# Performance work log

Hardware: AMD Instinct MI355X
Metric: run time of the kernel (lower is better)

Reference implementation:

```python
import jax, jax.numpy as jnp
import numpy as np

B, C, T = 8, 256, 8192
CALC, H = 256, 4
D = CALC // H  # head dim = 64
EPS = 1e-5


def setup_inputs() -> dict:
    key = jax.random.key(0)
    ks = jax.random.split(key, 5)
    return {
        "x": jax.random.normal(ks[0], (B, C, T), dtype=jnp.float32),
        "W_prenet": jax.random.normal(ks[1], (3 * CALC, C), dtype=jnp.float32) * 0.05,
        "W_proj": jax.random.normal(ks[2], (C, CALC), dtype=jnp.float32) * 0.05,
        "b_proj": jax.random.normal(ks[3], (C,), dtype=jnp.float32) * 0.05,
        "scale": jax.random.normal(ks[4], (1,), dtype=jnp.float32),
        "gamma": jnp.ones((C,), dtype=jnp.float32),
        "beta": jnp.zeros((C,), dtype=jnp.float32),
    }


def reference(x, W_prenet, W_proj, b_proj, scale, gamma, beta):
    residual = x
    # 1x1 conv prenet: [B, 3*CALC, T]
    h = jnp.einsum('oc,bct->bot', W_prenet, x)
    # split heads: channels grouped as H blocks of 3*D, then chunk into q/k/v of D each
    h = h.reshape(B, H, 3 * D, T)
    q = h[:, :, :D, :]            # [B,H,D,T]
    k = h[:, :, D:2 * D, :]
    v = h[:, :, 2 * D:, :]
    # softmax over time on keys (with the module's +1e-5 shift)
    k = jax.nn.softmax(k + EPS, axis=3)
    # keys @ values^T : [B,H,Dk,Dv]
    kv = jnp.einsum('bhdt,bhet->bhde', k, v)
    # kv^T @ queries  : [B,H,Dv,T]
    ctx = jnp.einsum('bhde,bhdt->bhet', kv, q)
    ctx = ctx.reshape(B, CALC, T)
    # 1x1 conv projection + bias
    out = jnp.einsum('oc,bct->bot', W_proj, ctx) + b_proj[None, :, None]
    out = scale * out  # learnable scalar gate
    # dropout is identity in eval mode
    out = out + residual
    # LayerNorm over channel axis with per-channel affine
    mean = jnp.mean(out, axis=1, keepdims=True)
    var = jnp.var(out, axis=1, keepdims=True)
    out = (out - mean) * jax.lax.rsqrt(var + EPS)
    out = out * gamma[None, :, None] + beta[None, :, None]
    return out
```

## Files before the change

### kernel.cpp

```cpp
#include <hip/hip_runtime.h>
#include <hip/hip_bf16.h>
#include <math.h>

#define BB 8
#define CC 256
#define TT 8192
#define EPSF 1e-5f

typedef short v8s __attribute__((ext_vector_type(8)));
typedef float v4f __attribute__((ext_vector_type(4)));

#define MFMA(a, b, c) __builtin_amdgcn_mfma_f32_16x16x32_bf16((a), (b), (c), 0, 0, 0)


#define OFF_WKV 0
#define OFF_WPJ 65536
#define OFF_UPART 98304
#define OFF_ZPART 8486912
#define OFF_KV 8617984
#define OFF_PT 8749056
#define OFF_MBF 9011200

__device__ __forceinline__ unsigned short f2bf(float f) {
  __hip_bfloat16 h = __float2bfloat16(f);
  return __builtin_bit_cast(unsigned short, h);
}
__device__ __forceinline__ float bf2f(unsigned short u) {
  return __bfloat162float(__builtin_bit_cast(__hip_bfloat16, u));
}
__device__ __forceinline__ unsigned int pack2(float lo, float hi) {
  return (unsigned int)f2bf(lo) | ((unsigned int)f2bf(hi) << 16);
}

__global__ void k0_pack(const float* __restrict__ Wpre,
                        const float* __restrict__ Wproj,
                        float* __restrict__ ws) {
  const int r = blockIdx.x;
  const int c = threadIdx.x;
  if (r < 512) {
    const int h = r >> 7, type = (r >> 6) & 1, d = r & 63;
    const int src = h * 192 + 64 + type * 64 + d;
    ((unsigned short*)(ws + OFF_WKV))[r * 256 + c] = f2bf(Wpre[(size_t)src * 256 + c]);
  } else {
    const int rr = r - 512;
    ((unsigned short*)(ws + OFF_WPJ))[rr * 256 + c] = f2bf(Wproj[(size_t)rr * 256 + c]);
  }
}

__global__ __launch_bounds__(512, 2) void k1_kv(const float* __restrict__ x,
                                                float* __restrict__ ws) {
  __shared__ unsigned short lds[20480];

  const int tid = threadIdx.x;
  const int w = tid >> 6, lane = tid & 63, q = lane >> 4, cl = lane & 15;
  const int h = w >> 1, type = w & 1;
  const int bi = blockIdx.x;
  const int b = bi >> 6, chunk = bi & 63;
  const int t0 = chunk * 128;
  const float* xb = x + (size_t)b * (CC * TT);
  const unsigned short* wkv =
      (const unsigned short*)(ws + OFF_WKV) + (size_t)((h * 2 + type) * 64) * 256;
  unsigned short* ekb = &lds[h * 5120];
  unsigned short* vbb = &lds[h * 5120 + 2560];

  v4f Uacc[2][4];
#pragma unroll
  for (int i = 0; i < 2; ++i)
#pragma unroll
    for (int j = 0; j < 4; ++j) Uacc[i][j] = (v4f){0.f, 0.f, 0.f, 0.f};
  float zacc[4][4];
#pragma unroll
  for (int i = 0; i < 4; ++i)
#pragma unroll
    for (int j = 0; j < 4; ++j) zacc[i][j] = 0.f;

  const int c0 = (tid & 127) * 2;
  const int th = tid >> 7;
  unsigned int* l32 = (unsigned int*)lds;

  for (int sub = 0; sub < 2; ++sub) {
    const int ts = t0 + sub * 64;
    {
      const float* xpA = xb + (size_t)c0 * TT + ts + th * 16;
      const float* xpB = xpA + TT;
      const int cw = c0 >> 1;
#pragma unroll
      for (int k = 0; k < 4; ++k) {
        const float4 va = reinterpret_cast<const float4*>(xpA)[k];
        const float4 vb = reinterpret_cast<const float4*>(xpB)[k];
        const int tb = th * 16 + k * 4;
        l32[(tb + 0) * 132 + cw] = pack2(va.x, vb.x);
        l32[(tb + 1) * 132 + cw] = pack2(va.y, vb.y);
        l32[(tb + 2) * 132 + cw] = pack2(va.z, vb.z);
        l32[(tb + 3) * 132 + cw] = pack2(va.w, vb.w);
      }
    }
    __syncthreads();

    v4f acc[4][4];
#pragma unroll
    for (int i = 0; i < 4; ++i)
#pragma unroll
      for (int j = 0; j < 4; ++j) acc[i][j] = (v4f){0.f, 0.f, 0.f, 0.f};
#pragma unroll
    for (int ks = 0; ks < 8; ++ks) {
      v8s af[4], bfu[4];
#pragma unroll
      for (int rt = 0; rt < 4; ++rt)
        af[rt] = *(const v8s*)(wkv + (size_t)(rt * 16 + cl) * 256 + ks * 32 + q * 8);
#pragma unroll
      for (int ct = 0; ct < 4; ++ct)
        bfu[ct] = *(const v8s*)&lds[(ct * 16 + cl) * 264 + ks * 32 + q * 8];
#pragma unroll
      for (int rt = 0; rt < 4; ++rt)
#pragma unroll
        for (int ct = 0; ct < 4; ++ct)
          acc[rt][ct] = MFMA(af[rt], bfu[ct], acc[rt][ct]);
    }
    __syncthreads();

#pragma unroll
    for (int hp = 0; hp < 2; ++hp) {
      if (type == 0) {
#pragma unroll
        for (int rt = 0; rt < 4; ++rt)
#pragma unroll
          for (int cc = 0; cc < 2; ++cc) {
            const int ct = hp * 2 + cc;
#pragma unroll
            for (int reg = 0; reg < 4; ++reg) {
              const float e = __expf(acc[rt][ct][reg]);
              zacc[rt][reg] += e;
              ekb[(rt * 16 + q * 4 + reg) * 40 + cc * 16 + cl] = f2bf(e);
            }
          }
      } else {
#pragma unroll
        for (int rt = 0; rt < 4; ++rt)
#pragma unroll
          for (int cc = 0; cc < 2; ++cc) {
            const int ct = hp * 2 + cc;
#pragma unroll
            for (int reg = 0; reg < 4; ++reg)
              vbb[(rt * 16 + q * 4 + reg) * 40 + cc * 16 + cl] =
                  f2bf(acc[rt][ct][reg]);
          }
      }
      __syncthreads();
      {
        const int du0 = type * 32;
        v8s afu[2], bfu[4];
#pragma unroll
        for (int ur = 0; ur < 2; ++ur)
          afu[ur] = *(const v8s*)&ekb[(du0 + ur * 16 + cl) * 40 + q * 8];
#pragma unroll
        for (int uc = 0; uc < 4; ++uc)
          bfu[uc] = *(const v8s*)&vbb[(uc * 16 + cl) * 40 + q * 8];
#pragma unroll
        for (int ur = 0; ur < 2; ++ur)
#pragma unroll
          for (int uc = 0; uc < 4; ++uc)
            Uacc[ur][uc] = MFMA(afu[ur], bfu[uc], Uacc[ur][uc]);
      }
      __syncthreads();
    }
  }

  if (type == 0) {
#pragma unroll
    for (int m = 1; m < 16; m <<= 1)
#pragma unroll
      for (int rt = 0; rt < 4; ++rt)
#pragma unroll
        for (int reg = 0; reg < 4; ++reg)
          zacc[rt][reg] += __shfl_xor(zacc[rt][reg], m, 64);
    if (cl == 0) {
      for (int rt = 0; rt < 4; ++rt)
        for (int reg = 0; reg < 4; ++reg)
          ws[OFF_ZPART + (size_t)bi * 256 + h * 64 + rt * 16 + q * 4 + reg] =
              zacc[rt][reg];
    }
  }
  float* Up = ws + OFF_UPART + (size_t)bi * 16384 + h * 4096;
#pragma unroll
  for (int ur = 0; ur < 2; ++ur)
#pragma unroll
    for (int uc = 0; uc < 4; ++uc)
#pragma unroll
      for (int reg = 0; reg < 4; ++reg)
        Up[(type * 32 + ur * 16 + q * 4 + reg) * 64 + uc * 16 + cl] =
            Uacc[ur][uc][reg];
}

__global__ void k2_reduce_kv(float* __restrict__ ws) {
  const int bi = blockIdx.x;
  const int bh = bi >> 4, j = bi & 15;
  const int b = bh >> 2, h = bh & 3;
  const int tid = threadIdx.x;

  __shared__ float zinv[64];
  if (tid < 64) {
    float z = 0.f;
    for (int cb = 0; cb < 64; ++cb)
      z += ws[OFF_ZPART + (size_t)(b * 64 + cb) * 256 + h * 64 + tid];
    zinv[tid] = 1.0f / z;
  }
  __syncthreads();

  const int idx = j * 256 + tid;
  const int d = idx >> 6;
  float s = 0.f;
  for (int cb = 0; cb < 64; ++cb)
    s += ws[OFF_UPART + (size_t)(b * 64 + cb) * 16384 + h * 4096 + idx];
  ws[OFF_KV + (size_t)(b * 4 + h) * 4096 + idx] = s * zinv[d];
}

__global__ void k3a_P(const float* __restrict__ Wpre, float* __restrict__ ws) {
  const int bi = blockIdx.x;
  const int b = bi >> 8, he = bi & 255;
  const int h = he >> 6, e = he & 63;
  const int c = threadIdx.x;
  const float* kvp = ws + OFF_KV + (size_t)(b * 4 + h) * 4096;
  float acc = 0.f;
#pragma unroll 8
  for (int d = 0; d < 64; ++d)
    acc += kvp[d * 64 + e] * Wpre[(size_t)(h * 192 + d) * 256 + c];
  ((unsigned short*)(ws + OFF_PT))[(size_t)b * 65536 + (size_t)c * 256 + he] =
      f2bf(acc);
}

__global__ __launch_bounds__(256, 2) void k3b_M(const float* __restrict__ scale,
                                                float* __restrict__ ws) {
  const int bi = blockIdx.x;
  const int b = bi >> 4, cg = (bi >> 2) & 3, rg = bi & 3;
  const int tid = threadIdx.x, w = tid >> 6, lane = tid & 63, q = lane >> 4,
            cl = lane & 15;
  const unsigned short* wpj = (const unsigned short*)(ws + OFF_WPJ);
  const unsigned short* pt =
      (const unsigned short*)(ws + OFF_PT) + (size_t)b * 65536;
  v4f acc[4];
#pragma unroll
  for (int j = 0; j < 4; ++j) acc[j] = (v4f){0.f, 0.f, 0.f, 0.f};
#pragma unroll
  for (int ks = 0; ks < 8; ++ks) {
    const v8s af = *(const v8s*)(wpj + (size_t)(rg * 64 + w * 16 + cl) * 256 +
                                 ks * 32 + q * 8);
    v8s bfu[4];
#pragma unroll
    for (int ct = 0; ct < 4; ++ct)
      bfu[ct] = *(const v8s*)(pt + (size_t)(cg * 64 + ct * 16 + cl) * 256 +
                              ks * 32 + q * 8);
#pragma unroll
    for (int ct = 0; ct < 4; ++ct) acc[ct] = MFMA(af, bfu[ct], acc[ct]);
  }
  const float s = scale[0];
  unsigned short* mbf = (unsigned short*)(ws + OFF_MBF);
#pragma unroll
  for (int ct = 0; ct < 4; ++ct)
#pragma unroll
    for (int reg = 0; reg < 4; ++reg) {
      const int o = rg * 64 + w * 16 + q * 4 + reg;
      const int c = cg * 64 + ct * 16 + cl;
      mbf[((size_t)b * 256 + o) * 256 + c] = f2bf(s * acc[ct][reg]);
    }
}

__global__ __launch_bounds__(256, 2) void k4_proj_ln(
    const float* __restrict__ x, const float* __restrict__ bproj,
    const float* __restrict__ scale, const float* __restrict__ gamma,
    const float* __restrict__ beta, const float* __restrict__ ws,
    float* __restrict__ out) {
  __shared__ unsigned short xs[32 * 264];
  __shared__ float red1[128], red2[128], muA[32], rsA[32];
  const int bi = blockIdx.x, b = bi >> 8, tc = bi & 255;
  const int tg0 = tc * 32;
  const int tid = threadIdx.x, w = tid >> 6, lane = tid & 63, q = lane >> 4,
            cl = lane & 15;
  const float* xb = x + (size_t)b * (CC * TT);

  {
    const int c0 = (tid & 127) * 2;
    const int th = tid >> 7;
    const float* xpA = xb + (size_t)c0 * TT + tg0 + th * 16;
    const float* xpB = xpA + TT;
    unsigned int* x32 = (unsigned int*)xs;
    const int cw = c0 >> 1;
#pragma unroll
    for (int k = 0; k < 4; ++k) {
      const float4 va = reinterpret_cast<const float4*>(xpA)[k];
      const float4 vb = reinterpret_cast<const float4*>(xpB)[k];
      const int tb = th * 16 + k * 4;
      x32[(tb + 0) * 132 + cw] = pack2(va.x, vb.x);
      x32[(tb + 1) * 132 + cw] = pack2(va.y, vb.y);
      x32[(tb + 2) * 132 + cw] = pack2(va.z, vb.z);
      x32[(tb + 3) * 132 + cw] = pack2(va.w, vb.w);
    }
  }
  __syncthreads();

  const unsigned short* mbf =
      (const unsigned short*)(ws + OFF_MBF) + (size_t)b * 65536;
  v4f acc[4][2];
#pragma unroll
  for (int i = 0; i < 4; ++i)
#pragma unroll
    for (int j = 0; j < 2; ++j) acc[i][j] = (v4f){0.f, 0.f, 0.f, 0.f};
#pragma unroll
  for (int ks = 0; ks < 8; ++ks) {
    v8s af[4], bfu[2];
#pragma unroll
    for (int rt = 0; rt < 4; ++rt)
      af[rt] = *(const v8s*)(mbf + (size_t)(w * 64 + rt * 16 + cl) * 256 +
                             ks * 32 + q * 8);
#pragma unroll
    for (int ct = 0; ct < 2; ++ct)
      bfu[ct] = *(const v8s*)&xs[(ct * 16 + cl) * 264 + ks * 32 + q * 8];
#pragma unroll
    for (int rt = 0; rt < 4; ++rt)
#pragma unroll
      for (int ct = 0; ct < 2; ++ct)
        acc[rt][ct] = MFMA(af[rt], bfu[ct], acc[rt][ct]);
  }

  const float s = scale[0];
#pragma unroll
  for (int rt = 0; rt < 4; ++rt)
#pragma unroll
    for (int reg = 0; reg < 4; ++reg) {
      const int o = w * 64 + rt * 16 + q * 4 + reg;
      const float sb = s * bproj[o];
#pragma unroll
      for (int ct = 0; ct < 2; ++ct) {
        const int tl = ct * 16 + cl;
        acc[rt][ct][reg] += sb + bf2f(xs[tl * 264 + o]);
      }
    }

#pragma unroll
  for (int ct = 0; ct < 2; ++ct) {
    float s1 = 0.f, s2 = 0.f;
#pragma unroll
    for (int rt = 0; rt < 4; ++rt)
#pragma unroll
      for (int reg = 0; reg < 4; ++reg) {
        const float v = acc[rt][ct][reg];
        s1 += v;
        s2 += v * v;
      }
    s1 += __shfl_xor(s1, 16, 64);
    s1 += __shfl_xor(s1, 32, 64);
    s2 += __shfl_xor(s2, 16, 64);
    s2 += __shfl_xor(s2, 32, 64);
    if (q == 0) {
      red1[w * 32 + ct * 16 + cl] = s1;
      red2[w * 32 + ct * 16 + cl] = s2;
    }
  }
  __syncthreads();
  if (tid < 32) {
    const float s1 = red1[tid] + red1[32 + tid] + red1[64 + tid] + red1[96 + tid];
    const float s2 = red2[tid] + red2[32 + tid] + red2[64 + tid] + red2[96 + tid];
    const float mu = s1 * (1.f / 256.f);
    const float var = s2 * (1.f / 256.f) - mu * mu;
    muA[tid] = mu;
    rsA[tid] = rsqrtf(var + EPSF);
  }
  __syncthreads();

  float* ob = out + (size_t)b * (CC * TT) + tg0;
#pragma unroll
  for (int rt = 0; rt < 4; ++rt)
#pragma unroll
    for (int reg = 0; reg < 4; ++reg) {
      const int o = w * 64 + rt * 16 + q * 4 + reg;
      const float g = gamma[o], bt = beta[o];
#pragma unroll
      for (int ct = 0; ct < 2; ++ct) {
        const int tl = ct * 16 + cl;
        ob[(size_t)o * TT + tl] = (acc[rt][ct][reg] - muA[tl]) * rsA[tl] * g + bt;
      }
    }
}

extern "C" void kernel_launch(void* const* d_in, const int* in_sizes, int n_in,
                              void* d_out, int out_size, void* d_ws,
                              size_t ws_size, hipStream_t stream) {
  (void)in_sizes; (void)n_in; (void)out_size; (void)ws_size;
  const float* x = (const float*)d_in[0];
  const float* Wpre = (const float*)d_in[1];
  const float* Wproj = (const float*)d_in[2];
  const float* bproj = (const float*)d_in[3];
  const float* scale = (const float*)d_in[4];
  const float* gamma = (const float*)d_in[5];
  const float* beta = (const float*)d_in[6];
  float* out = (float*)d_out;
  float* ws = (float*)d_ws;

  hipLaunchKernelGGL(k0_pack, dim3(768), dim3(256), 0, stream, Wpre, Wproj, ws);
  hipLaunchKernelGGL(k1_kv, dim3(512), dim3(512), 0, stream, x, ws);
  hipLaunchKernelGGL(k2_reduce_kv, dim3(512), dim3(256), 0, stream, ws);
  hipLaunchKernelGGL(k3a_P, dim3(BB * 256), dim3(256), 0, stream, Wpre, ws);
  hipLaunchKernelGGL(k3b_M, dim3(128), dim3(256), 0, stream, scale, ws);
  hipLaunchKernelGGL(k4_proj_ln, dim3(BB * 128 * 2), dim3(256), 0, stream, x,
                     bproj, scale, gamma, beta, ws, out);
}
```

Baseline: 236.0 us.

## Double-buffer x tiles in kv kernel and split waves by time half

The key/value kernel now processes 256 time steps per block, in four sub-tiles, instead of 128 in two, halving the grid to 256 blocks. Global loads of the next x tile are issued before the MFMA work on the current tile, and the tile is written into a second LDS buffer afterwards, so loads overlap compute. Each wave now computes both K and V for one head over half the time columns, which removes the type-divergent branch and some barriers. The reduction kernel sums half as many partials. The cost is a much larger LDS footprint (about 146 KB per block) and more registers, which lowers occupancy and may prevent the requested two blocks per CU.

New measurement: 287.6 us. 21.8% more time.

```diff
diff --git a/kernel.cpp b/kernel.cpp
--- a/kernel.cpp
+++ b/kernel.cpp
@@ -16,10 +16,10 @@
 #define OFF_WKV 0
 #define OFF_WPJ 65536
 #define OFF_UPART 98304
-#define OFF_ZPART 8486912
-#define OFF_KV 8617984
-#define OFF_PT 8749056
-#define OFF_MBF 9011200
+#define OFF_ZPART 4292608
+#define OFF_KV 4423680
+#define OFF_PT 4554752
+#define OFF_MBF 4816896
 
 __device__ __forceinline__ unsigned short f2bf(float f) {
   __hip_bfloat16 h = __float2bfloat16(f);
@@ -49,19 +49,21 @@
 
 __global__ __launch_bounds__(512, 2) void k1_kv(const float* __restrict__ x,
                                                 float* __restrict__ ws) {
-  __shared__ unsigned short lds[20480];
+  __shared__ unsigned short lds[74752];
 
   const int tid = threadIdx.x;
   const int w = tid >> 6, lane = tid & 63, q = lane >> 4, cl = lane & 15;
-  const int h = w >> 1, type = w & 1;
+  const int h = w >> 1, thalf = w & 1;
+  const int tw0 = thalf * 32;
   const int bi = blockIdx.x;
-  const int b = bi >> 6, chunk = bi & 63;
-  const int t0 = chunk * 128;
+  const int b = bi >> 5, chunk = bi & 31;
+  const int t0 = chunk * 256;
   const float* xb = x + (size_t)b * (CC * TT);
-  const unsigned short* wkv =
-      (const unsigned short*)(ws + OFF_WKV) + (size_t)((h * 2 + type) * 64) * 256;
-  unsigned short* ekb = &lds[h * 5120];
-  unsigned short* vbb = &lds[h * 5120 + 2560];
+  const unsigned short* wk =
+      (const unsigned short*)(ws + OFF_WKV) + (size_t)((h * 2 + 0) * 64) * 256;
+  const unsigned short* wv =
+      (const unsigned short*)(ws + OFF_WKV) + (size_t)((h * 2 + 1) * 64) * 256;
+  unsigned short* evh = &lds[33792 + (h * 2) * 5120];
 
   v4f Uacc[2][4];
 #pragma unroll
@@ -76,110 +78,131 @@
 
   const int c0 = (tid & 127) * 2;
   const int th = tid >> 7;
+  const int cw = tid & 127;
   unsigned int* l32 = (unsigned int*)lds;
 
-  for (int sub = 0; sub < 2; ++sub) {
-    const int ts = t0 + sub * 64;
+  {
+    const float* xpA = xb + (size_t)c0 * TT + t0 + th * 16;
+    const float* xpB = xpA + TT;
+#pragma unroll
+    for (int k = 0; k < 4; ++k) {
+      const float4 va = reinterpret_cast<const float4*>(xpA)[k];
+      const float4 vb4 = reinterpret_cast<const float4*>(xpB)[k];
+      const int tb = th * 16 + k * 4;
+      l32[(tb + 0) * 132 + cw] = pack2(va.x, vb4.x);
+      l32[(tb + 1) * 132 + cw] = pack2(va.y, vb4.y);
+      l32[(tb + 2) * 132 + cw] = pack2(va.z, vb4.z);
+      l32[(tb + 3) * 132 + cw] = pack2(va.w, vb4.w);
+    }
+  }
+
+#pragma unroll
+  for (int sub = 0; sub < 4; ++sub) {
+    const int cur = sub & 1;
+    const unsigned short* xsr = &lds[cur * 16896];
+    __syncthreads();
+
+    float4 nxA[4], nxB[4];
+    if (sub < 3) {
+      const float* xpA = xb + (size_t)c0 * TT + (t0 + (sub + 1) * 64) + th * 16;
+      const float* xpB = xpA + TT;
+#pragma unroll
+      for (int k = 0; k < 4; ++k) {
+        nxA[k] = reinterpret_cast<const float4*>(xpA)[k];
+        nxB[k] = reinterpret_cast<const float4*>(xpB)[k];
+      }
+    }
+
+    v4f kacc[4][2], vacc[4][2];
+#pragma unroll
+    for (int i = 0; i < 4; ++i)
+#pragma unroll
+      for (int j = 0; j < 2; ++j) {
+        kacc[i][j] = (v4f){0.f, 0.f, 0.f, 0.f};
+        vacc[i][j] = (v4f){0.f, 0.f, 0.f, 0.f};
+      }
+#pragma unroll
+    for (int ks = 0; ks < 8; ++ks) {
+      v8s afk[4], afv[4], bfu[2];
+#pragma unroll
+      for (int rt = 0; rt < 4; ++rt)
+        afk[rt] = *(const v8s*)(wk + (size_t)(rt * 16 + cl) * 256 + ks * 32 + q * 8);
+#pragma unroll
+      for (int rt = 0; rt < 4; ++rt)
+        afv[rt] = *(const v8s*)(wv + (size_t)(rt * 16 + cl) * 256 + ks * 32 + q * 8);
+#pragma unroll
+      for (int ct = 0; ct < 2; ++ct)
+        bfu[ct] = *(const v8s*)&xsr[(tw0 + ct * 16 + cl) * 264 + ks * 32 + q * 8];
+#pragma unroll
+      for (int rt = 0; rt < 4; ++rt)
+#pragma unroll
+        for (int ct = 0; ct < 2; ++ct) {
+          kacc[rt][ct] = MFMA(afk[rt], bfu[ct], kacc[rt][ct]);
+          vacc[rt][ct] = MFMA(afv[rt], bfu[ct], vacc[rt][ct]);
+        }
+    }
+
     {
-      const float* xpA = xb + (size_t)c0 * TT + ts + th * 16;
-      const float* xpB = xpA + TT;
-      const int cw = c0 >> 1;
+      unsigned short* ek = evh + thalf * 5120;
+      unsigned short* vbf = ek + 2560;
+#pragma unroll
+      for (int rt = 0; rt < 4; ++rt)
+#pragma unroll
+        for (int ct = 0; ct < 2; ++ct)
+#pragma unroll
+          for (int reg = 0; reg < 4; ++reg) {
+            const int row = rt * 16 + q * 4 + reg;
+            const float e = __expf(kacc[rt][ct][reg]);
+            zacc[rt][reg] += e;
+            ek[row * 40 + ct * 16 + cl] = f2bf(e);
+            vbf[row * 40 + ct * 16 + cl] = f2bf(vacc[rt][ct][reg]);
+          }
+    }
+    __syncthreads();
+
+#pragma unroll
+    for (int s = 0; s < 2; ++s) {
+      const unsigned short* eks = evh + s * 5120;
+      const unsigned short* vbs = eks + 2560;
+      v8s afu[2], bfv[4];
+#pragma unroll
+      for (int ur = 0; ur < 2; ++ur)
+        afu[ur] = *(const v8s*)&eks[(tw0 + ur * 16 + cl) * 40 + q * 8];
+#pragma unroll
+      for (int uc = 0; uc < 4; ++uc)
+        bfv[uc] = *(const v8s*)&vbs[(uc * 16 + cl) * 40 + q * 8];
+#pragma unroll
+      for (int ur = 0; ur < 2; ++ur)
+#pragma unroll
+        for (int uc = 0; uc < 4; ++uc)
+          Uacc[ur][uc] = MFMA(afu[ur], bfv[uc], Uacc[ur][uc]);
+    }
+
+    if (sub < 3) {
+      unsigned int* xw = l32 + (cur ^ 1) * 8448;
 #pragma unroll
       for (int k = 0; k < 4; ++k) {
-        const float4 va = reinterpret_cast<const float4*>(xpA)[k];
-        const float4 vb = reinterpret_cast<const float4*>(xpB)[k];
         const int tb = th * 16 + k * 4;
-        l32[(tb + 0) * 132 + cw] = pack2(va.x, vb.x);
-        l32[(tb + 1) * 132 + cw] = pack2(va.y, vb.y);
-        l32[(tb + 2) * 132 + cw] = pack2(va.z, vb.z);
-        l32[(tb + 3) * 132 + cw] = pack2(va.w, vb.w);
-      }
-    }
-    __syncthreads();
-
-    v4f acc[4][4];
-#pragma unroll
-    for (int i = 0; i < 4; ++i)
-#pragma unroll
-      for (int j = 0; j < 4; ++j) acc[i][j] = (v4f){0.f, 0.f, 0.f, 0.f};
-#pragma unroll
-    for (int ks = 0; ks < 8; ++ks) {
-      v8s af[4], bfu[4];
-#pragma unroll
-      for (int rt = 0; rt < 4; ++rt)
-        af[rt] = *(const v8s*)(wkv + (size_t)(rt * 16 + cl) * 256 + ks * 32 + q * 8);
-#pragma unroll
-      for (int ct = 0; ct < 4; ++ct)
-        bfu[ct] = *(const v8s*)&lds[(ct * 16 + cl) * 264 + ks * 32 + q * 8];
-#pragma unroll
-      for (int rt = 0; rt < 4; ++rt)
-#pragma unroll
-        for (int ct = 0; ct < 4; ++ct)
-          acc[rt][ct] = MFMA(af[rt], bfu[ct], acc[rt][ct]);
-    }
-    __syncthreads();
-
-#pragma unroll
-    for (int hp = 0; hp < 2; ++hp) {
-      if (type == 0) {
-#pragma unroll
-        for (int rt = 0; rt < 4; ++rt)
-#pragma unroll
-          for (int cc = 0; cc < 2; ++cc) {
-            const int ct = hp * 2 + cc;
-#pragma unroll
-            for (int reg = 0; reg < 4; ++reg) {
-              const float e = __expf(acc[rt][ct][reg]);
-              zacc[rt][reg] += e;
-              ekb[(rt * 16 + q * 4 + reg) * 40 + cc * 16 + cl] = f2bf(e);
-            }
-          }
-      } else {
-#pragma unroll
-        for (int rt = 0; rt < 4; ++rt)
-#pragma unroll
-          for (int cc = 0; cc < 2; ++cc) {
-            const int ct = hp * 2 + cc;
-#pragma unroll
-            for (int reg = 0; reg < 4; ++reg)
-              vbb[(rt * 16 + q * 4 + reg) * 40 + cc * 16 + cl] =
-                  f2bf(acc[rt][ct][reg]);
-          }
-      }
-      __syncthreads();
-      {
-        const int du0 = type * 32;
-        v8s afu[2], bfu[4];
-#pragma unroll
-        for (int ur = 0; ur < 2; ++ur)
-          afu[ur] = *(const v8s*)&ekb[(du0 + ur * 16 + cl) * 40 + q * 8];
-#pragma unroll
-        for (int uc = 0; uc < 4; ++uc)
-          bfu[uc] = *(const v8s*)&vbb[(uc * 16 + cl) * 40 + q * 8];
-#pragma unroll
-        for (int ur = 0; ur < 2; ++ur)
-#pragma unroll
-          for (int uc = 0; uc < 4; ++uc)
-            Uacc[ur][uc] = MFMA(afu[ur], bfu[uc], Uacc[ur][uc]);
-      }
-      __syncthreads();
-    }
-  }
-
-  if (type == 0) {
-#pragma unroll
-    for (int m = 1; m < 16; m <<= 1)
-#pragma unroll
-      for (int rt = 0; rt < 4; ++rt)
-#pragma unroll
-        for (int reg = 0; reg < 4; ++reg)
-          zacc[rt][reg] += __shfl_xor(zacc[rt][reg], m, 64);
-    if (cl == 0) {
-      for (int rt = 0; rt < 4; ++rt)
-        for (int reg = 0; reg < 4; ++reg)
-          ws[OFF_ZPART + (size_t)bi * 256 + h * 64 + rt * 16 + q * 4 + reg] =
-              zacc[rt][reg];
-    }
+        xw[(tb + 0) * 132 + cw] = pack2(nxA[k].x, nxB[k].x);
+        xw[(tb + 1) * 132 + cw] = pack2(nxA[k].y, nxB[k].y);
+        xw[(tb + 2) * 132 + cw] = pack2(nxA[k].z, nxB[k].z);
+        xw[(tb + 3) * 132 + cw] = pack2(nxA[k].w, nxB[k].w);
+      }
+    }
+  }
+
+#pragma unroll
+  for (int m = 1; m < 16; m <<= 1)
+#pragma unroll
+    for (int rt = 0; rt < 4; ++rt)
+#pragma unroll
+      for (int reg = 0; reg < 4; ++reg)
+        zacc[rt][reg] += __shfl_xor(zacc[rt][reg], m, 64);
+  if (cl == 0) {
+    for (int rt = 0; rt < 4; ++rt)
+      for (int reg = 0; reg < 4; ++reg)
+        ws[OFF_ZPART + (size_t)bi * 512 + w * 64 + rt * 16 + q * 4 + reg] =
+            zacc[rt][reg];
   }
   float* Up = ws + OFF_UPART + (size_t)bi * 16384 + h * 4096;
 #pragma unroll
@@ -188,7 +211,7 @@
     for (int uc = 0; uc < 4; ++uc)
 #pragma unroll
       for (int reg = 0; reg < 4; ++reg)
-        Up[(type * 32 + ur * 16 + q * 4 + reg) * 64 + uc * 16 + cl] =
+        Up[(tw0 + ur * 16 + q * 4 + reg) * 64 + uc * 16 + cl] =
             Uacc[ur][uc][reg];
 }
 
@@ -201,8 +224,11 @@
   __shared__ float zinv[64];
   if (tid < 64) {
     float z = 0.f;
-    for (int cb = 0; cb < 64; ++cb)
-      z += ws[OFF_ZPART + (size_t)(b * 64 + cb) * 256 + h * 64 + tid];
+#pragma unroll 4
+    for (int cb = 0; cb < 32; ++cb) {
+      const size_t base = OFF_ZPART + (size_t)(b * 32 + cb) * 512;
+      z += ws[base + (h * 2 + 0) * 64 + tid] + ws[base + (h * 2 + 1) * 64 + tid];
+    }
     zinv[tid] = 1.0f / z;
   }
   __syncthreads();
@@ -210,8 +236,9 @@
   const int idx = j * 256 + tid;
   const int d = idx >> 6;
   float s = 0.f;
-  for (int cb = 0; cb < 64; ++cb)
-    s += ws[OFF_UPART + (size_t)(b * 64 + cb) * 16384 + h * 4096 + idx];
+#pragma unroll 4
+  for (int cb = 0; cb < 32; ++cb)
+    s += ws[OFF_UPART + (size_t)(b * 32 + cb) * 16384 + h * 4096 + idx];
   ws[OFF_KV + (size_t)(b * 4 + h) * 4096 + idx] = s * zinv[d];
 }
 
@@ -397,7 +424,7 @@
   float* ws = (float*)d_ws;
 
   hipLaunchKernelGGL(k0_pack, dim3(768), dim3(256), 0, stream, Wpre, Wproj, ws);
-  hipLaunchKernelGGL(k1_kv, dim3(512), dim3(512), 0, stream, x, ws);
+  hipLaunchKernelGGL(k1_kv, dim3(256), dim3(512), 0, stream, x, ws);
   hipLaunchKernelGGL(k2_reduce_kv, dim3(512), dim3(256), 0, stream, ws);
   hipLaunchKernelGGL(k3a_P, dim3(BB * 256), dim3(256), 0, stream, Wpre, ws);
   hipLaunchKernelGGL(k3b_M, dim3(128), dim3(256), 0, stream, scale, ws);
```
